# Performance work log

Measured on AMD Instinct MI355X. Metric: run time of the kernel, lower is better.

The kernel has to match this reference:

```python
import jax, jax.numpy as jnp
import numpy as np

NMS_THRESH = 0.5
SCORE_THRESH = 0.2
MAX_SUBJECT = 15
MAX_OBJECT = 15
B, NS, NO = 32, 512, 512


def _make_boxes(k, b, n):
    u = jax.random.uniform(k, (b, n, 4))
    xy = u[..., :2] * 1000.0          # top-left corner
    wh = u[..., 2:] * 200.0 + 1.0     # positive width/height
    return jnp.concatenate([xy, xy + wh], axis=-1)  # valid xyxy boxes


def setup_inputs() -> dict:
    key = jax.random.key(0)
    ks = jax.random.split(key, 6)
    return {
        "subj_boxes": _make_boxes(ks[0], B, NS),
        "subj_scores": jax.random.uniform(ks[1], (B, NS)),
        "subj_labels": jax.random.randint(ks[2], (B, NS), 0, 30, dtype=jnp.int32),
        "obj_boxes": _make_boxes(ks[3], B, NO),
        "obj_scores": jax.random.uniform(ks[4], (B, NO)),
        "obj_labels": jax.random.randint(ks[5], (B, NO), 0, 30, dtype=jnp.int32),
    }


def reference(subj_boxes, subj_scores, subj_labels, obj_boxes, obj_scores, obj_labels):
    # concat subject + object detections per image, as in preprocess()
    boxes = jnp.concatenate([subj_boxes, obj_boxes], axis=1)    # [B,N,4]
    scores = jnp.concatenate([subj_scores, obj_scores], axis=1) # [B,N]
    labels = jnp.concatenate([subj_labels, obj_labels], axis=1) # [B,N]
    b, n = scores.shape
    is_subj = jnp.arange(n) < subj_boxes.shape[1]               # [N]

    # sort by score descending (matches the argsort after NMS; greedy NMS
    # preserves this ordering among survivors)
    order = jnp.argsort(-scores, axis=1)
    boxes = jnp.take_along_axis(boxes, order[..., None], axis=1)
    scores = jnp.take_along_axis(scores, order, axis=1)
    labels = jnp.take_along_axis(labels, order, axis=1)
    is_subj = jnp.take(is_subj, order)                          # [B,N]

    active = scores >= SCORE_THRESH

    # torchvision batched_nms: offset boxes per class so distinct classes
    # never overlap (comparisons only -> no gradient path)
    max_coord = jax.lax.stop_gradient(jnp.max(boxes))
    ob = boxes + labels.astype(boxes.dtype)[..., None] * (max_coord + 1.0)

    # pairwise IoU [B,N,N]
    area = (ob[..., 2] - ob[..., 0]) * (ob[..., 3] - ob[..., 1])
    lt = jnp.maximum(ob[:, :, None, :2], ob[:, None, :, :2])
    rb = jnp.minimum(ob[:, :, None, 2:], ob[:, None, :, 2:])
    wh = jnp.clip(rb - lt, 0.0)
    inter = wh[..., 0] * wh[..., 1]
    iou = inter / (area[:, :, None] + area[:, None, :] - inter)

    later = jnp.arange(n)[None, :] > jnp.arange(n)[:, None]     # strictly lower-score

    def body(i, suppressed):  # greedy NMS, vectorized over batch
        keep_i = active[:, i] & ~suppressed[:, i]
        return suppressed | (keep_i[:, None] & (iou[:, i, :] > NMS_THRESH) & later[i])

    suppressed = jax.lax.fori_loop(0, n, body, jnp.zeros((b, n), dtype=bool))
    kept = active & ~suppressed

    # split survivors into subjects / objects, keep top max_subject/max_object
    neg = jnp.finfo(scores.dtype).min
    sub_key = jnp.where(kept & is_subj, scores, neg)
    obj_key = jnp.where(kept & ~is_subj, scores, neg)
    sv, si = jax.lax.top_k(sub_key, MAX_SUBJECT)
    ov, oi = jax.lax.top_k(obj_key, MAX_OBJECT)
    idx = jnp.concatenate([si, oi], axis=1)                     # [B,K]
    valid = jnp.concatenate([sv, ov], axis=1) > neg             # [B,K]

    out_boxes = jnp.take_along_axis(boxes, idx[..., None], axis=1) * valid[..., None]
    out_scores = jnp.take_along_axis(scores, idx, axis=1) * valid
    out_labels = jnp.where(valid, jnp.take_along_axis(labels, idx, axis=1), -1)
    num_subjects = jnp.sum(sv > neg, axis=1)
    return out_boxes, out_scores, out_labels, num_subjects, valid
```

## Files before the change

kernel.cpp:

```cpp
#include <hip/hip_runtime.h>
#include <stdint.h>

#define BQ    32
#define NSUB  512
#define NDET  1024
#define NCLS  30
#define KSLOT 30
#define BCAP  96

#pragma clang fp contract(off)

typedef unsigned long long u64;

__global__ __launch_bounds__(512) void bucket_kernel(
    const float* __restrict__ sb, const float* __restrict__ ss,
    const int*   __restrict__ sl,
    const float* __restrict__ ob, const float* __restrict__ os,
    const int*   __restrict__ ol,
    float* __restrict__ pmax, int* __restrict__ cnts,
    u64* __restrict__ bkeys, float4* __restrict__ bboxes)
{
    const int b = blockIdx.x, t = threadIdx.x;
    const int lane = t & 63, w = t >> 6;
    __shared__ int   lcnt[NCLS];
    __shared__ float wred[8];

    if (t < NCLS) lcnt[t] = 0;

    float4 bxs = *(const float4*)(sb + (size_t)(b * NSUB + t) * 4);
    float4 bxo = *(const float4*)(ob + (size_t)(b * NSUB + t) * 4);
    float scs = ss[b * NSUB + t];  int lbs = sl[b * NSUB + t];
    float sco = os[b * NSUB + t];  int lbo = ol[b * NSUB + t];

    float m = fmaxf(fmaxf(fmaxf(bxs.x, bxs.y), fmaxf(bxs.z, bxs.w)),
                    fmaxf(fmaxf(bxo.x, bxo.y), fmaxf(bxo.z, bxo.w)));
    for (int off = 32; off; off >>= 1) m = fmaxf(m, __shfl_xor(m, off));
    if (lane == 0) wred[w] = m;
    __syncthreads();
    if (t == 0) {
        float mm = wred[0];
        for (int i = 1; i < 8; ++i) mm = fmaxf(mm, wred[i]);
        pmax[b] = mm;
    }

    if (scs >= 0.2f) {
        int pos = atomicAdd(&lcnt[lbs], 1);
        if (pos < BCAP) {
            size_t s = ((size_t)b * NCLS + lbs) * BCAP + pos;
            bkeys[s]  = ((u64)__float_as_uint(scs) << 32) | (u64)(1023 - t);
            bboxes[s] = bxs;
        }
    }
    if (sco >= 0.2f) {
        int pos = atomicAdd(&lcnt[lbo], 1);
        if (pos < BCAP) {
            size_t s = ((size_t)b * NCLS + lbo) * BCAP + pos;
            bkeys[s]  = ((u64)__float_as_uint(sco) << 32) | (u64)(1023 - (512 + t));
            bboxes[s] = bxo;
        }
    }
    __syncthreads();
    if (t < NCLS) {
        int c = lcnt[t];
        cnts[b * NCLS + t] = (c < BCAP) ? c : BCAP;
    }
}

__global__ __launch_bounds__(64) void nms_class_kernel(
    const float* __restrict__ pmax, const int* __restrict__ cnts,
    const u64* __restrict__ bkeys, const float4* __restrict__ bboxes,
    u64* __restrict__ subk, u64* __restrict__ objk)
{
#pragma clang fp contract(off)
    const int c    = blockIdx.x;
    const int b    = blockIdx.y;
    const int lane = threadIdx.x;

    __shared__ u64    keyarr[BCAP];
    __shared__ u64    skey[BCAP];
    __shared__ float4 bxs4[BCAP];

    const size_t base = (size_t)b * NCLS + c;

    u64    K1 = bkeys[base * BCAP + lane];
    float4 B1 = bboxes[base * BCAP + lane];
    u64 K2 = 0; float4 B2 = make_float4(0.f, 0.f, 0.f, 0.f);
    if (lane < BCAP - 64) {
        K2 = bkeys[base * BCAP + 64 + lane];
        B2 = bboxes[base * BCAP + 64 + lane];
    }
    const int cnt = cnts[base];
    float pv = pmax[lane & 31];
    for (int off = 32; off; off >>= 1) pv = fmaxf(pv, __shfl_xor(pv, off));
    const float mco  = pv + 1.0f;
    const float offc = (float)c * mco;

    keyarr[lane] = K1;
    if (lane < BCAP - 64) keyarr[64 + lane] = K2;
    __threadfence_block();

    {
        int r = 0;
        for (int l = 0; l < cnt; ++l) r += (keyarr[l] > K1) ? 1 : 0;
        if (lane < cnt) { skey[r] = K1; bxs4[r] = B1; }
    }
    if (cnt > 64) {
        int e = 64 + lane;
        int r = 0;
        for (int l = 0; l < cnt; ++l) r += (keyarr[l] > K2) ? 1 : 0;
        if (e < cnt) { skey[r] = K2; bxs4[r] = B2; }
    }
    __threadfence_block();

    const int  lim1  = (cnt < 64) ? cnt : 64;
    const bool have1 = (lane < lim1);
    u64 SK1 = have1 ? skey[lane] : 0;
    int idx1 = 1023 - (int)(unsigned)(SK1 & 0xffffffffull);
    float4 bj1 = have1 ? bxs4[lane] : make_float4(0.f, 0.f, 0.f, 0.f);
    const bool have2 = (64 + lane) < cnt;
    u64 SK2 = 0; int idx2 = 0; float4 bj2 = make_float4(0.f, 0.f, 0.f, 0.f);
    if (cnt > 64) {
        SK2 = have2 ? skey[64 + lane] : 0;
        idx2 = 1023 - (int)(unsigned)(SK2 & 0xffffffffull);
        if (have2) bj2 = bxs4[64 + lane];
    }

    float j0 = bj1.x + offc, j1 = bj1.y + offc;
    float j2v = bj1.z + offc, j3 = bj1.w + offc;
    float aj = (j2v - j0) * (j3 - j1);
    u64 ov = 0;
    for (int l = 0; l < lim1; ++l) {
        float4 bl = bxs4[l];
        float i0 = bl.x + offc, i1 = bl.y + offc;
        float i2 = bl.z + offc, i3 = bl.w + offc;
        float ai = (i2 - i0) * (i3 - i1);
        if (have1 && l < lane) {
            float ltx = fmaxf(i0, j0), lty = fmaxf(i1, j1);
            float rbx = fminf(i2, j2v), rby = fminf(i3, j3);
            float wx = fmaxf(rbx - ltx, 0.0f), wy = fmaxf(rby - lty, 0.0f);
            float inter = wx * wy;
            float iou = inter / ((ai + aj) - inter);
            if (iou > 0.5f) ov |= (1ull << l);
        }
    }
    bool sup1 = !have1;
    for (int l = 0; l < lim1; ++l) {
        u64 bal = __ballot(sup1);
        if (!((bal >> l) & 1ull)) sup1 = sup1 || (((ov >> l) & 1ull) != 0ull);
    }
    const bool kept1 = have1 && !sup1;
    const u64 keptA = __ballot(kept1);

    bool kept2 = false;
    if (cnt > 64) {
        float k0 = bj2.x + offc, k1 = bj2.y + offc;
        float k2 = bj2.z + offc, k3 = bj2.w + offc;
        float ak = (k2 - k0) * (k3 - k1);
        bool sup2 = !have2;
        for (int l = 0; l < 64; ++l) {
            if ((keptA >> l) & 1ull) {
                float4 bl = bxs4[l];
                float i0 = bl.x + offc, i1 = bl.y + offc;
                float i2 = bl.z + offc, i3 = bl.w + offc;
                float ai = (i2 - i0) * (i3 - i1);
                if (!sup2) {
                    float ltx = fmaxf(i0, k0), lty = fmaxf(i1, k1);
                    float rbx = fminf(i2, k2), rby = fminf(i3, k3);
                    float wx = fmaxf(rbx - ltx, 0.0f), wy = fmaxf(rby - lty, 0.0f);
                    float inter = wx * wy;
                    float iou = inter / ((ai + ak) - inter);
                    if (iou > 0.5f) sup2 = true;
                }
            }
        }
        u64 ov2 = 0;
        const int lim2 = cnt - 64;
        for (int l = 0; l < lim2; ++l) {
            float4 bl = bxs4[64 + l];
            float i0 = bl.x + offc, i1 = bl.y + offc;
            float i2 = bl.z + offc, i3 = bl.w + offc;
            float ai = (i2 - i0) * (i3 - i1);
            if (have2 && l < lane) {
                float ltx = fmaxf(i0, k0), lty = fmaxf(i1, k1);
                float rbx = fminf(i2, k2), rby = fminf(i3, k3);
                float wx = fmaxf(rbx - ltx, 0.0f), wy = fmaxf(rby - lty, 0.0f);
                float inter = wx * wy;
                float iou = inter / ((ai + ak) - inter);
                if (iou > 0.5f) ov2 |= (1ull << l);
            }
        }
        for (int l = 0; l < lim2; ++l) {
            u64 bal = __ballot(sup2);
            if (!((bal >> l) & 1ull)) sup2 = sup2 || (((ov2 >> l) & 1ull) != 0ull);
        }
        kept2 = have2 && !sup2;
    }

    const bool s1 = kept1 && (idx1 < NSUB), o1 = kept1 && (idx1 >= NSUB);
    const bool s2 = kept2 && (idx2 < NSUB), o2 = kept2 && (idx2 >= NSUB);
    const u64 mS1 = __ballot(s1), mS2 = __ballot(s2);
    const u64 mO1 = __ballot(o1), mO2 = __ballot(o2);
    const u64 ltm = (1ull << lane) - 1ull;
    u64* subp = subk + base * 15;
    u64* objp = objk + base * 15;
    if (s1) { int p = (int)__popcll(mS1 & ltm); if (p < 15) subp[p] = SK1; }
    if (s2) { int p = (int)__popcll(mS1) + (int)__popcll(mS2 & ltm); if (p < 15) subp[p] = SK2; }
    if (o1) { int p = (int)__popcll(mO1 & ltm); if (p < 15) objp[p] = SK1; }
    if (o2) { int p = (int)__popcll(mO1) + (int)__popcll(mO2 & ltm); if (p < 15) objp[p] = SK2; }
    int tS = (int)(__popcll(mS1) + __popcll(mS2)); if (tS > 15) tS = 15;
    int tO = (int)(__popcll(mO1) + __popcll(mO2)); if (tO > 15) tO = 15;
    if (lane >= tS && lane < 15) subp[lane] = 0;
    if (lane >= tO && lane < 15) objp[lane] = 0;
}

__global__ __launch_bounds__(64) void select_kernel(
    const float* __restrict__ sb, const int* __restrict__ sl,
    const float* __restrict__ ob, const int* __restrict__ ol,
    const u64* __restrict__ subk, const u64* __restrict__ objk,
    float* __restrict__ out)
{
    const int b    = blockIdx.x;
    const int side = blockIdx.y;
    const int lane = threadIdx.x;

    float* outB = out;
    float* outS = out + BQ * KSLOT * 4;
    float* outL = outS + BQ * KSLOT;
    float* outN = outL + BQ * KSLOT;
    float* outV = outN + BQ;

    const u64* src = (side ? objk : subk) + (size_t)b * NCLS * 15;
    u64 kk[8];
    #pragma unroll
    for (int i = 0; i < 8; ++i) {
        int p = lane + 64 * i;
        kk[i] = (p < NCLS * 15) ? src[p] : 0;
    }
    int nvalid = 0;
    for (int r = 0; r < 15; ++r) {
        u64 lm = 0; int li = 0;
        #pragma unroll
        for (int i = 0; i < 8; ++i) if (kk[i] > lm) { lm = kk[i]; li = i; }
        u64 gm = lm;
        for (int off = 32; off; off >>= 1) {
            u64 o = __shfl_xor(gm, off);
            if (o > gm) gm = o;
        }
        int p = b * KSLOT + (side ? (15 + r) : r);
        if (gm == 0) {
            if (lane == 0) {
                *(float4*)(outB + (size_t)p * 4) = make_float4(0.f, 0.f, 0.f, 0.f);
                outS[p] = 0.0f; outL[p] = -1.0f; outV[p] = 0.0f;
            }
        } else {
            u64 win = __ballot(lm == gm);
            int wl = (int)__ffsll(win) - 1;
            if (lane == wl) {
                kk[li] = 0;
                int idx = 1023 - (int)(unsigned)(gm & 0xffffffffull);
                float score = __uint_as_float((unsigned)(gm >> 32));
                float4 bx; int lb;
                if (idx < NSUB) {
                    bx = *(const float4*)(sb + (size_t)(b * NSUB + idx) * 4);
                    lb = sl[b * NSUB + idx];
                } else {
                    bx = *(const float4*)(ob + (size_t)(b * NSUB + idx - NSUB) * 4);
                    lb = ol[b * NSUB + idx - NSUB];
                }
                *(float4*)(outB + (size_t)p * 4) = bx;
                outS[p] = score;
                outL[p] = (float)lb;
                outV[p] = 1.0f;
            }
            nvalid++;
        }
    }
    if (side == 0 && lane == 0) outN[b] = (float)nvalid;
}

extern "C" void kernel_launch(void* const* d_in, const int* in_sizes, int n_in,
                              void* d_out, int out_size, void* d_ws, size_t ws_size,
                              hipStream_t stream) {
    const float* sb = (const float*)d_in[0];
    const float* ss = (const float*)d_in[1];
    const int*   sl = (const int*)d_in[2];
    const float* ob = (const float*)d_in[3];
    const float* os = (const float*)d_in[4];
    const int*   ol = (const int*)d_in[5];

    float*  pmax   = (float*)d_ws;
    int*    cnts   = (int*)((char*)d_ws + 256);
    u64*    bkeys  = (u64*)((char*)d_ws + 8192);
    float4* bboxes = (float4*)((char*)d_ws + 745472);
    u64*    subk   = (u64*)((char*)d_ws + 2220032);
    u64*    objk   = subk + (size_t)BQ * NCLS * 15;

    bucket_kernel<<<dim3(BQ), dim3(512), 0, stream>>>(
        sb, ss, sl, ob, os, ol, pmax, cnts, bkeys, bboxes);
    nms_class_kernel<<<dim3(NCLS, BQ), dim3(64), 0, stream>>>(
        pmax, cnts, bkeys, bboxes, subk, objk);
    select_kernel<<<dim3(BQ, 2), dim3(64), 0, stream>>>(
        sb, sl, ob, ol, subk, objk, (float*)d_out);
}
```

Measured before the change: 87.72 us.

## Spread bucketing over many small blocks using global atomics and memset

The bucketing kernel now runs 512 blocks of 64 threads, one detection per thread, instead of one 512-thread block per image. Per-class counters and the global coordinate max move from shared memory to global atomics, with a memset clearing them first. The NMS kernel clamps the count itself and reads the single global max instead of reducing 32 per-image maxima. This aims to spread the first stage across more compute units, at the cost of an extra memset launch and contention on global atomics.

```diff
diff --git a/kernel.cpp b/kernel.cpp
--- a/kernel.cpp
+++ b/kernel.cpp
@@ -12,62 +12,44 @@
 
 typedef unsigned long long u64;
 
-__global__ __launch_bounds__(512) void bucket_kernel(
+__global__ __launch_bounds__(64) void bucket_kernel(
     const float* __restrict__ sb, const float* __restrict__ ss,
     const int*   __restrict__ sl,
     const float* __restrict__ ob, const float* __restrict__ os,
     const int*   __restrict__ ol,
-    float* __restrict__ pmax, int* __restrict__ cnts,
+    unsigned* __restrict__ pmaxu, int* __restrict__ cnts,
     u64* __restrict__ bkeys, float4* __restrict__ bboxes)
 {
-    const int b = blockIdx.x, t = threadIdx.x;
-    const int lane = t & 63, w = t >> 6;
-    __shared__ int   lcnt[NCLS];
-    __shared__ float wred[8];
-
-    if (t < NCLS) lcnt[t] = 0;
-
-    float4 bxs = *(const float4*)(sb + (size_t)(b * NSUB + t) * 4);
-    float4 bxo = *(const float4*)(ob + (size_t)(b * NSUB + t) * 4);
-    float scs = ss[b * NSUB + t];  int lbs = sl[b * NSUB + t];
-    float sco = os[b * NSUB + t];  int lbo = ol[b * NSUB + t];
-
-    float m = fmaxf(fmaxf(fmaxf(bxs.x, bxs.y), fmaxf(bxs.z, bxs.w)),
-                    fmaxf(fmaxf(bxo.x, bxo.y), fmaxf(bxo.z, bxo.w)));
+    const int g = blockIdx.x * 64 + threadIdx.x;
+    const int b = g >> 10;
+    const int i = g & 1023;
+
+    float sc; int lb; float4 bx;
+    if (i < NSUB) {
+        sc = ss[b * NSUB + i];  lb = sl[b * NSUB + i];
+        bx = *(const float4*)(sb + (size_t)(b * NSUB + i) * 4);
+    } else {
+        int u = i - NSUB;
+        sc = os[b * NSUB + u];  lb = ol[b * NSUB + u];
+        bx = *(const float4*)(ob + (size_t)(b * NSUB + u) * 4);
+    }
+
+    float m = fmaxf(fmaxf(bx.x, bx.y), fmaxf(bx.z, bx.w));
     for (int off = 32; off; off >>= 1) m = fmaxf(m, __shfl_xor(m, off));
-    if (lane == 0) wred[w] = m;
-    __syncthreads();
-    if (t == 0) {
-        float mm = wred[0];
-        for (int i = 1; i < 8; ++i) mm = fmaxf(mm, wred[i]);
-        pmax[b] = mm;
-    }
-
-    if (scs >= 0.2f) {
-        int pos = atomicAdd(&lcnt[lbs], 1);
+    if (threadIdx.x == 0) atomicMax(pmaxu, __float_as_uint(m));
+
+    if (sc >= 0.2f) {
+        int pos = atomicAdd(&cnts[b * NCLS + lb], 1);
         if (pos < BCAP) {
-            size_t s = ((size_t)b * NCLS + lbs) * BCAP + pos;
-            bkeys[s]  = ((u64)__float_as_uint(scs) << 32) | (u64)(1023 - t);
-            bboxes[s] = bxs;
-        }
-    }
-    if (sco >= 0.2f) {
-        int pos = atomicAdd(&lcnt[lbo], 1);
-        if (pos < BCAP) {
-            size_t s = ((size_t)b * NCLS + lbo) * BCAP + pos;
-            bkeys[s]  = ((u64)__float_as_uint(sco) << 32) | (u64)(1023 - (512 + t));
-            bboxes[s] = bxo;
-        }
-    }
-    __syncthreads();
-    if (t < NCLS) {
-        int c = lcnt[t];
-        cnts[b * NCLS + t] = (c < BCAP) ? c : BCAP;
+            size_t s = ((size_t)b * NCLS + lb) * BCAP + pos;
+            bkeys[s]  = ((u64)__float_as_uint(sc) << 32) | (u64)(1023 - i);
+            bboxes[s] = bx;
+        }
     }
 }
 
 __global__ __launch_bounds__(64) void nms_class_kernel(
-    const float* __restrict__ pmax, const int* __restrict__ cnts,
+    const unsigned* __restrict__ pmaxu, const int* __restrict__ cnts,
     const u64* __restrict__ bkeys, const float4* __restrict__ bboxes,
     u64* __restrict__ subk, u64* __restrict__ objk)
 {
@@ -89,10 +71,8 @@
         K2 = bkeys[base * BCAP + 64 + lane];
         B2 = bboxes[base * BCAP + 64 + lane];
     }
-    const int cnt = cnts[base];
-    float pv = pmax[lane & 31];
-    for (int off = 32; off; off >>= 1) pv = fmaxf(pv, __shfl_xor(pv, off));
-    const float mco  = pv + 1.0f;
+    int cnt = cnts[base]; if (cnt > BCAP) cnt = BCAP;
+    const float mco  = __uint_as_float(pmaxu[0]) + 1.0f;
     const float offc = (float)c * mco;
 
     keyarr[lane] = K1;
@@ -288,17 +268,18 @@
     const float* os = (const float*)d_in[4];
     const int*   ol = (const int*)d_in[5];
 
-    float*  pmax   = (float*)d_ws;
-    int*    cnts   = (int*)((char*)d_ws + 256);
-    u64*    bkeys  = (u64*)((char*)d_ws + 8192);
-    float4* bboxes = (float4*)((char*)d_ws + 745472);
-    u64*    subk   = (u64*)((char*)d_ws + 2220032);
-    u64*    objk   = subk + (size_t)BQ * NCLS * 15;
-
-    bucket_kernel<<<dim3(BQ), dim3(512), 0, stream>>>(
-        sb, ss, sl, ob, os, ol, pmax, cnts, bkeys, bboxes);
+    unsigned* pmaxu  = (unsigned*)d_ws;
+    int*      cnts   = (int*)((char*)d_ws + 128);
+    u64*      bkeys  = (u64*)((char*)d_ws + 8192);
+    float4*   bboxes = (float4*)((char*)d_ws + 745472);
+    u64*      subk   = (u64*)((char*)d_ws + 2220032);
+    u64*      objk   = subk + (size_t)BQ * NCLS * 15;
+
+    hipMemsetAsync(d_ws, 0, 4096, stream);
+    bucket_kernel<<<dim3(512), dim3(64), 0, stream>>>(
+        sb, ss, sl, ob, os, ol, pmaxu, cnts, bkeys, bboxes);
     nms_class_kernel<<<dim3(NCLS, BQ), dim3(64), 0, stream>>>(
-        pmax, cnts, bkeys, bboxes, subk, objk);
+        pmaxu, cnts, bkeys, bboxes, subk, objk);
     select_kernel<<<dim3(BQ, 2), dim3(64), 0, stream>>>(
         sb, sl, ob, ol, subk, objk, (float*)d_out);
 }
```

Measured after the change: 97.78 us. 11.5% more time.
